# Optimization experiments

Measured on AMD Instinct MI355X. Metric: run time of the kernel, lower is better.

Reference implementation:

```python
import jax, jax.numpy as jnp
import numpy as np

NOISE_EPS = 0.01
TOP_K = 2


def setup_inputs() -> dict:
    key = jax.random.key(0)
    k1, k2, k3, k4 = jax.random.split(key, 4)
    B, S, D, E = 4, 4096, 2048, 64
    x = jax.random.normal(k1, (B, S, D), dtype=jnp.float32)
    raw_noise = jax.random.normal(k2, (B, S, E), dtype=jnp.float32)
    # gating_mlp: single Linear(D -> E), init std=0.02, zero bias
    W_gate = 0.02 * jax.random.normal(k3, (E, D), dtype=jnp.float32)
    b_gate = jnp.zeros((E,), dtype=jnp.float32)
    # noise_projection: Linear(D -> E, bias=False), init std=1/sqrt(D)
    W_noise = (1.0 / np.sqrt(D)) * jax.random.normal(k4, (E, D), dtype=jnp.float32)
    return {"x": x, "raw_noise": raw_noise, "W_gate": W_gate, "b_gate": b_gate, "W_noise": W_noise}


def reference(x, raw_noise, W_gate, b_gate, W_noise):
    # gate logits: [B,S,E]
    logits = jnp.einsum("bsd,ed->bse", x, W_gate) + b_gate
    # noisy top-k routing (training path)
    noise_stddev = jax.nn.softplus(jnp.einsum("bsd,ed->bse", x, W_noise)) + NOISE_EPS
    noisy = logits + raw_noise * noise_stddev
    top_v, top_i = jax.lax.top_k(noisy, TOP_K)            # [B,S,K]
    top_p = jax.nn.softmax(top_v.astype(jnp.float32), axis=-1).astype(noisy.dtype)
    B, S, E = noisy.shape
    T = B * S
    flat_logits = noisy.reshape(T, E)
    flat_i = top_i.reshape(T, TOP_K)
    flat_p = top_p.reshape(T, TOP_K)
    sparse = jnp.zeros((T, E), dtype=noisy.dtype).at[jnp.arange(T)[:, None], flat_i].set(flat_p)
    # aux load-balancing loss
    indicator = (sparse > 0.0).astype(jnp.float32)
    fraction_routed = indicator.sum(axis=0) / T           # f_e
    router_probs = jax.nn.softmax(flat_logits.astype(jnp.float32), axis=-1)
    avg_prob = router_probs.mean(axis=0)                  # p_e
    aux_loss = jnp.sum(fraction_routed * avg_prob) * E
    return sparse.reshape(B, S, E), aux_loss.astype(noisy.dtype)
```

## Files before the change

kernel.cpp:

```cpp
#include <hip/hip_runtime.h>
#include <math.h>

#define TOK 16384
#define DD  2048
#define EE  64
#define MT  32
#define BK  128
#define NKC 8
#define LDA 136
#define XREG (MT * LDA)

typedef _Float16 half4v __attribute__((ext_vector_type(4)));
typedef _Float16 half8  __attribute__((ext_vector_type(8)));
typedef float    floatx4 __attribute__((ext_vector_type(4)));

__global__ void build_wf(const float* __restrict__ Wg, const float* __restrict__ Wn,
                         _Float16* __restrict__ wf) {
  int tid  = blockIdx.x * 256 + threadIdx.x;
  int lane = tid & 63;
  int kc   = (tid >> 6) & 63;
  int ct   = tid >> 12;
  int col  = (ct & 3) * 16 + (lane & 15);
  int k    = kc * 32 + (lane >> 4) * 8;
  const float* W = (ct < 4) ? Wg : Wn;
  const float* src = W + (size_t)col * DD + k;
  float4 a = *reinterpret_cast<const float4*>(src);
  float4 b = *reinterpret_cast<const float4*>(src + 4);
  float v[8] = {a.x, a.y, a.z, a.w, b.x, b.y, b.z, b.w};
  half8 hi, lo;
#pragma unroll
  for (int j = 0; j < 8; ++j) {
    _Float16 h = (_Float16)v[j];
    hi[j] = h;
    lo[j] = (_Float16)(v[j] - (float)h);
  }
  size_t base = (((size_t)(ct * 64 + kc) * 2 + 0) * 64 + lane) * 8;
  *reinterpret_cast<half8*>(wf + base)       = hi;
  *reinterpret_cast<half8*>(wf + base + 512) = lo;
}

#define STAGE(BUF, P0, P1, P2, P3)                                              \
  {                                                                             \
    float4 pav[4] = {P0, P1, P2, P3};                                           \
    _Float16* xh = xs + ((g * 2 + (BUF)) * 2 + 0) * XREG + stok * LDA + skof;   \
    _Float16* xl = xh + XREG;                                                   \
    _Pragma("unroll")                                                           \
    for (int j = 0; j < 4; ++j) {                                               \
      float v[4] = {pav[j].x, pav[j].y, pav[j].z, pav[j].w};                    \
      half4v hi, lo;                                                            \
      _Pragma("unroll")                                                         \
      for (int jj = 0; jj < 4; ++jj) {                                          \
        _Float16 h = (_Float16)v[jj];                                           \
        hi[jj] = h;                                                             \
        lo[jj] = (_Float16)(v[jj] - (float)h);                                  \
      }                                                                         \
      *reinterpret_cast<half4v*>(xh + j * 32) = hi;                             \
      *reinterpret_cast<half4v*>(xl + j * 32) = lo;                             \
    }                                                                           \
  }

#define SUBK(KK, SC, SP, DOPF)                                                  \
  {                                                                             \
    half8 Ah[2], Al[2];                                                         \
    _Pragma("unroll")                                                           \
    for (int mt = 0; mt < 2; ++mt) {                                            \
      Ah[mt] = *reinterpret_cast<const half8*>(xsh + (mt * 16) * LDA + (KK) * 32); \
      Al[mt] = *reinterpret_cast<const half8*>(xsl + (mt * 16) * LDA + (KK) * 32); \
    }                                                                           \
    if (DOPF) {                                                                 \
      const int ck = g * 32 + kc * 4 + (KK) + 1;                                \
      _Pragma("unroll")                                                         \
      for (int nt = 0; nt < 2; ++nt) {                                          \
        const int ct = w4 + nt * 4;                                             \
        _Pragma("unroll")                                                       \
        for (int s = 0; s < 2; ++s)                                             \
          SP[nt][s] = wfp[((size_t)(ct * 64 + ck) * 2 + s) * 64 + l];           \
      }                                                                         \
    }                                                                           \
    _Pragma("unroll")                                                           \
    for (int mt = 0; mt < 2; ++mt)                                              \
      _Pragma("unroll")                                                         \
      for (int nt = 0; nt < 2; ++nt)                                            \
        acc[mt][nt] = __builtin_amdgcn_mfma_f32_16x16x32_f16(Ah[mt], SC[nt][0], acc[mt][nt], 0, 0, 0); \
    _Pragma("unroll")                                                           \
    for (int mt = 0; mt < 2; ++mt)                                              \
      _Pragma("unroll")                                                         \
      for (int nt = 0; nt < 2; ++nt)                                            \
        acc[mt][nt] = __builtin_amdgcn_mfma_f32_16x16x32_f16(Ah[mt], SC[nt][1], acc[mt][nt], 0, 0, 0); \
    _Pragma("unroll")                                                           \
    for (int mt = 0; mt < 2; ++mt)                                              \
      _Pragma("unroll")                                                         \
      for (int nt = 0; nt < 2; ++nt)                                            \
        acc[mt][nt] = __builtin_amdgcn_mfma_f32_16x16x32_f16(Al[mt], SC[nt][0], acc[mt][nt], 0, 0, 0); \
  }

__global__ __launch_bounds__(512, 4)
void gating_kernel(const float* __restrict__ x, const float* __restrict__ rn,
                   const _Float16* __restrict__ wf, const float* __restrict__ bg,
                   float* __restrict__ out,
                   float* __restrict__ cnt_g, float* __restrict__ psum_g) {
  __shared__ char smem[69632];
  _Float16* xs   = (_Float16*)smem;
  float*    Pacc = (float*)smem;
  float*    Vb   = (float*)(smem + 16384);
  float*    Eb   = (float*)(smem + 24832);
  float*    isum = (float*)(smem + 33280);
  int*      ti   = (int*)(smem + 33408);
  float*    tp   = (float*)(smem + 33664);

  const int t  = threadIdx.x;
  const int g  = t >> 8;
  const int tg = t & 255;
  const int w4 = tg >> 6;
  const int l  = t & 63;
  const int q  = l >> 4;
  const int cl = l & 15;
  const int c  = w4 * 16 + cl;
  const int t0 = blockIdx.x * MT;

  const int stok = tg >> 3;
  const int skof = (tg & 7) * 4;
  const float* xrow = x + (size_t)(t0 + stok) * DD + g * (NKC * BK) + skof;

  float bgv = 0.f;
  float rnv[2][4] = {{0.f,0.f,0.f,0.f},{0.f,0.f,0.f,0.f}};
  if (g == 0) {
    bgv = bg[c];
#pragma unroll
    for (int mt = 0; mt < 2; ++mt)
#pragma unroll
      for (int r = 0; r < 4; ++r)
        rnv[mt][r] = rn[(size_t)(t0 + mt * 16 + q * 4 + r) * EE + c];
  }

  floatx4 acc[2][2];
#pragma unroll
  for (int mt = 0; mt < 2; ++mt)
#pragma unroll
    for (int nt = 0; nt < 2; ++nt) acc[mt][nt] = (floatx4)0.f;

  const half8* wfp = (const half8*)wf;
  half8 Bs0[2][2], Bs1[2][2];

  {
    float4 a0 = *reinterpret_cast<const float4*>(xrow);
    float4 a1 = *reinterpret_cast<const float4*>(xrow + 32);
    float4 a2 = *reinterpret_cast<const float4*>(xrow + 64);
    float4 a3 = *reinterpret_cast<const float4*>(xrow + 96);
    STAGE(0, a0, a1, a2, a3)
    const int ck0 = g * 32;
#pragma unroll
    for (int nt = 0; nt < 2; ++nt) {
      const int ct = w4 + nt * 4;
#pragma unroll
      for (int s = 0; s < 2; ++s)
        Bs0[nt][s] = wfp[((size_t)(ct * 64 + ck0) * 2 + s) * 64 + l];
    }
  }

#pragma unroll 2
  for (int kc = 0; kc < NKC; ++kc) {
    const int cur = kc & 1;
    const bool more = (kc < NKC - 1);
    float4 p0, p1, p2, p3;
    if (more) {
      const float* xn = xrow + (kc + 1) * BK;
      p0 = *reinterpret_cast<const float4*>(xn);
      p1 = *reinterpret_cast<const float4*>(xn + 32);
      p2 = *reinterpret_cast<const float4*>(xn + 64);
      p3 = *reinterpret_cast<const float4*>(xn + 96);
    }
    asm volatile("s_waitcnt lgkmcnt(0)" ::: "memory");
    __builtin_amdgcn_s_barrier();

    const _Float16* xsh = xs + ((g * 2 + cur) * 2 + 0) * XREG + cl * LDA + q * 8;
    const _Float16* xsl = xsh + XREG;

    SUBK(0, Bs0, Bs1, 1)
    SUBK(1, Bs1, Bs0, 1)
    SUBK(2, Bs0, Bs1, 1)
    SUBK(3, Bs1, Bs0, more)

    if (more) {
      STAGE(cur ^ 1, p0, p1, p2, p3)
    }
  }

  __syncthreads();

  if (g == 1) {
#pragma unroll
    for (int mt = 0; mt < 2; ++mt)
#pragma unroll
      for (int nt = 0; nt < 2; ++nt)
#pragma unroll
        for (int r = 0; r < 4; ++r)
          Pacc[((((w4 * 2 + mt) * 2 + nt) * 4) + r) * 64 + l] = acc[mt][nt][r];
  }
  __syncthreads();

  if (g == 0) {
#pragma unroll
    for (int mt = 0; mt < 2; ++mt)
#pragma unroll
      for (int nt = 0; nt < 2; ++nt)
#pragma unroll
        for (int r = 0; r < 4; ++r)
          acc[mt][nt][r] += Pacc[((((w4 * 2 + mt) * 2 + nt) * 4) + r) * 64 + l];

#pragma unroll
    for (int mt = 0; mt < 2; ++mt)
#pragma unroll
      for (int r = 0; r < 4; ++r) {
        const int tk = mt * 16 + q * 4 + r;
        float gt = acc[mt][0][r] + bgv;
        float h  = acc[mt][1][r];
        float sp = (h > 20.f) ? h : log1pf(expf(h));
        float v  = gt + rnv[mt][r] * (sp + 0.01f);
        Vb[tk * 66 + c] = v;
        Eb[tk * 66 + c] = expf(v);
      }
  }
  __syncthreads();

  if (t < MT) {
    float v1 = -1e30f, v2 = -1e30f;
    int   i1 = 0, i2 = 0;
    float s = 0.f;
    for (int e = 0; e < EE; ++e) {
      float v = Vb[t * 66 + e];
      s += Eb[t * 66 + e];
      if (v > v1)      { v2 = v1; i2 = i1; v1 = v; i1 = e; }
      else if (v > v2) { v2 = v;  i2 = e; }
    }
    isum[t] = 1.f / s;
    ti[t * 2 + 0] = i1; ti[t * 2 + 1] = i2;
    float e2 = expf(v2 - v1);
    float dn = 1.f + e2;
    tp[t * 2 + 0] = 1.f / dn;
    tp[t * 2 + 1] = e2 / dn;
  }
  __syncthreads();

  {
    const int m  = t >> 4;
    const int c0 = (t & 15) * 4;
    const int i1 = ti[m * 2 + 0], i2 = ti[m * 2 + 1];
    const float p1 = tp[m * 2 + 0], p2 = tp[m * 2 + 1];
    float o[4];
#pragma unroll
    for (int j = 0; j < 4; ++j) {
      const int col = c0 + j;
      o[j] = (col == i1) ? p1 : ((col == i2) ? p2 : 0.f);
    }
    *reinterpret_cast<float4*>(out + (size_t)(t0 + m) * EE + c0) =
        make_float4(o[0], o[1], o[2], o[3]);
  }

  if (t < EE) {
    float s = 0.f;
    int   cn = 0;
#pragma unroll
    for (int m = 0; m < MT; ++m) {
      s  += Eb[m * 66 + t] * isum[m];
      cn += (ti[m * 2 + 0] == t) + (ti[m * 2 + 1] == t);
    }
    atomicAdd(&psum_g[t], s);
    atomicAdd(&cnt_g[t], (float)cn);
  }
}

__global__ void aux_kernel(const float* __restrict__ cnt_g,
                           const float* __restrict__ psum_g,
                           float* __restrict__ out) {
  int e = threadIdx.x;
  float v = cnt_g[e] * psum_g[e];
#pragma unroll
  for (int o = 32; o > 0; o >>= 1) v += __shfl_down(v, o);
  if (e == 0)
    out[(size_t)TOK * EE] = v * ((float)EE / ((float)TOK * (float)TOK));
}

extern "C" void kernel_launch(void* const* d_in, const int* in_sizes, int n_in,
                              void* d_out, int out_size, void* d_ws, size_t ws_size,
                              hipStream_t stream) {
  const float* x  = (const float*)d_in[0];
  const float* rn = (const float*)d_in[1];
  const float* Wg = (const float*)d_in[2];
  const float* bg = (const float*)d_in[3];
  const float* Wn = (const float*)d_in[4];
  float* out    = (float*)d_out;
  float* cnt_g  = (float*)d_ws;
  float* psum_g = cnt_g + EE;
  _Float16* wf  = (_Float16*)((float*)d_ws + 128);

  hipMemsetAsync(d_ws, 0, 2 * EE * sizeof(float), stream);
  build_wf<<<128, 256, 0, stream>>>(Wg, Wn, wf);
  gating_kernel<<<TOK / MT, 512, 0, stream>>>(x, rn, wf, bg, out, cnt_g, psum_g);
  aux_kernel<<<1, 64, 0, stream>>>(cnt_g, psum_g, out);
}
```

Before: 226.9 us.

## Halve token tile to 16 and drop weight register prefetch

Shrinks the per-block token tile from 32 to 16, which doubles the grid size, halves shared memory and raises the launch-bounds occupancy hint to 8. The double-buffered weight-fragment prefetch is replaced by loading the weights inside each sub-k step, and each thread now stages 8 contiguous floats of x. The workspace memset is folded into build_wf to drop a launch. The trade-off is that each block now reads the whole fp16 weight set for half as many tokens, doubling weight traffic, and weight load latency is no longer hidden by the prefetch.

```diff
diff --git a/kernel.cpp b/kernel.cpp
--- a/kernel.cpp
+++ b/kernel.cpp
@@ -4,19 +4,21 @@
 #define TOK 16384
 #define DD  2048
 #define EE  64
-#define MT  32
+#define MT  16
 #define BK  128
 #define NKC 8
 #define LDA 136
 #define XREG (MT * LDA)
+#define NBLK (TOK / MT)
 
 typedef _Float16 half4v __attribute__((ext_vector_type(4)));
 typedef _Float16 half8  __attribute__((ext_vector_type(8)));
 typedef float    floatx4 __attribute__((ext_vector_type(4)));
 
 __global__ void build_wf(const float* __restrict__ Wg, const float* __restrict__ Wn,
-                         _Float16* __restrict__ wf) {
-  int tid  = blockIdx.x * 256 + threadIdx.x;
+                         _Float16* __restrict__ wf, float* __restrict__ zws) {
+  if (blockIdx.x == 0 && threadIdx.x < 128) zws[threadIdx.x] = 0.f;
+  int tid  = blockIdx.x * 128 + threadIdx.x;
   int lane = tid & 63;
   int kc   = (tid >> 6) & 63;
   int ct   = tid >> 12;
@@ -39,13 +41,13 @@
   *reinterpret_cast<half8*>(wf + base + 512) = lo;
 }
 
-#define STAGE(BUF, P0, P1, P2, P3)                                              \
+#define STAGE(BUF, P0, P1)                                                      \
   {                                                                             \
-    float4 pav[4] = {P0, P1, P2, P3};                                           \
+    float4 pav[2] = {P0, P1};                                                   \
     _Float16* xh = xs + ((g * 2 + (BUF)) * 2 + 0) * XREG + stok * LDA + skof;   \
     _Float16* xl = xh + XREG;                                                   \
     _Pragma("unroll")                                                           \
-    for (int j = 0; j < 4; ++j) {                                               \
+    for (int j = 0; j < 2; ++j) {                                               \
       float v[4] = {pav[j].x, pav[j].y, pav[j].z, pav[j].w};                    \
       half4v hi, lo;                                                            \
       _Pragma("unroll")                                                         \
@@ -54,59 +56,48 @@
         hi[jj] = h;                                                             \
         lo[jj] = (_Float16)(v[jj] - (float)h);                                  \
       }                                                                         \
-      *reinterpret_cast<half4v*>(xh + j * 32) = hi;                             \
-      *reinterpret_cast<half4v*>(xl + j * 32) = lo;                             \
+      *reinterpret_cast<half4v*>(xh + j * 4) = hi;                              \
+      *reinterpret_cast<half4v*>(xl + j * 4) = lo;                              \
     }                                                                           \
   }
 
-#define SUBK(KK, SC, SP, DOPF)                                                  \
+#define SUBK(KK)                                                                \
   {                                                                             \
-    half8 Ah[2], Al[2];                                                         \
-    _Pragma("unroll")                                                           \
-    for (int mt = 0; mt < 2; ++mt) {                                            \
-      Ah[mt] = *reinterpret_cast<const half8*>(xsh + (mt * 16) * LDA + (KK) * 32); \
-      Al[mt] = *reinterpret_cast<const half8*>(xsl + (mt * 16) * LDA + (KK) * 32); \
+    half8 Ah = *reinterpret_cast<const half8*>(xsh + (KK) * 32);                \
+    half8 Al = *reinterpret_cast<const half8*>(xsl + (KK) * 32);                \
+    half8 Bv[2][2];                                                             \
+    const int ck = g * 32 + kc * 4 + (KK);                                      \
+    _Pragma("unroll")                                                           \
+    for (int nt = 0; nt < 2; ++nt) {                                            \
+      const int ct = w4 + nt * 4;                                               \
+      _Pragma("unroll")                                                         \
+      for (int s = 0; s < 2; ++s)                                               \
+        Bv[nt][s] = wfp[((size_t)(ct * 64 + ck) * 2 + s) * 64 + l];             \
     }                                                                           \
-    if (DOPF) {                                                                 \
-      const int ck = g * 32 + kc * 4 + (KK) + 1;                                \
-      _Pragma("unroll")                                                         \
-      for (int nt = 0; nt < 2; ++nt) {                                          \
-        const int ct = w4 + nt * 4;                                             \
-        _Pragma("unroll")                                                       \
-        for (int s = 0; s < 2; ++s)                                             \
-          SP[nt][s] = wfp[((size_t)(ct * 64 + ck) * 2 + s) * 64 + l];           \
-      }                                                                         \
-    }                                                                           \
-    _Pragma("unroll")                                                           \
-    for (int mt = 0; mt < 2; ++mt)                                              \
-      _Pragma("unroll")                                                         \
-      for (int nt = 0; nt < 2; ++nt)                                            \
-        acc[mt][nt] = __builtin_amdgcn_mfma_f32_16x16x32_f16(Ah[mt], SC[nt][0], acc[mt][nt], 0, 0, 0); \
-    _Pragma("unroll")                                                           \
-    for (int mt = 0; mt < 2; ++mt)                                              \
-      _Pragma("unroll")                                                         \
-      for (int nt = 0; nt < 2; ++nt)                                            \
-        acc[mt][nt] = __builtin_amdgcn_mfma_f32_16x16x32_f16(Ah[mt], SC[nt][1], acc[mt][nt], 0, 0, 0); \
-    _Pragma("unroll")                                                           \
-    for (int mt = 0; mt < 2; ++mt)                                              \
-      _Pragma("unroll")                                                         \
-      for (int nt = 0; nt < 2; ++nt)                                            \
-        acc[mt][nt] = __builtin_amdgcn_mfma_f32_16x16x32_f16(Al[mt], SC[nt][0], acc[mt][nt], 0, 0, 0); \
-  }
-
-__global__ __launch_bounds__(512, 4)
+    _Pragma("unroll")                                                           \
+    for (int nt = 0; nt < 2; ++nt)                                              \
+      acc[nt] = __builtin_amdgcn_mfma_f32_16x16x32_f16(Ah, Bv[nt][0], acc[nt], 0, 0, 0); \
+    _Pragma("unroll")                                                           \
+    for (int nt = 0; nt < 2; ++nt)                                              \
+      acc[nt] = __builtin_amdgcn_mfma_f32_16x16x32_f16(Ah, Bv[nt][1], acc[nt], 0, 0, 0); \
+    _Pragma("unroll")                                                           \
+    for (int nt = 0; nt < 2; ++nt)                                              \
+      acc[nt] = __builtin_amdgcn_mfma_f32_16x16x32_f16(Al, Bv[nt][0], acc[nt], 0, 0, 0); \
+  }
+
+__global__ __launch_bounds__(512, 8)
 void gating_kernel(const float* __restrict__ x, const float* __restrict__ rn,
                    const _Float16* __restrict__ wf, const float* __restrict__ bg,
                    float* __restrict__ out,
                    float* __restrict__ cnt_g, float* __restrict__ psum_g) {
-  __shared__ char smem[69632];
+  __shared__ char smem[34816];
   _Float16* xs   = (_Float16*)smem;
   float*    Pacc = (float*)smem;
-  float*    Vb   = (float*)(smem + 16384);
-  float*    Eb   = (float*)(smem + 24832);
-  float*    isum = (float*)(smem + 33280);
-  int*      ti   = (int*)(smem + 33408);
-  float*    tp   = (float*)(smem + 33664);
+  float*    Vb   = (float*)(smem + 8192);
+  float*    Eb   = (float*)(smem + 12416);
+  float*    isum = (float*)(smem + 16640);
+  int*      ti   = (int*)(smem + 16704);
+  float*    tp   = (float*)(smem + 16832);
 
   const int t  = threadIdx.x;
   const int g  = t >> 8;
@@ -118,57 +109,31 @@
   const int c  = w4 * 16 + cl;
   const int t0 = blockIdx.x * MT;
 
-  const int stok = tg >> 3;
-  const int skof = (tg & 7) * 4;
+  const int stok = tg >> 4;
+  const int skof = (tg & 15) * 8;
   const float* xrow = x + (size_t)(t0 + stok) * DD + g * (NKC * BK) + skof;
 
-  float bgv = 0.f;
-  float rnv[2][4] = {{0.f,0.f,0.f,0.f},{0.f,0.f,0.f,0.f}};
-  if (g == 0) {
-    bgv = bg[c];
-#pragma unroll
-    for (int mt = 0; mt < 2; ++mt)
-#pragma unroll
-      for (int r = 0; r < 4; ++r)
-        rnv[mt][r] = rn[(size_t)(t0 + mt * 16 + q * 4 + r) * EE + c];
-  }
-
-  floatx4 acc[2][2];
-#pragma unroll
-  for (int mt = 0; mt < 2; ++mt)
-#pragma unroll
-    for (int nt = 0; nt < 2; ++nt) acc[mt][nt] = (floatx4)0.f;
+  floatx4 acc[2];
+  acc[0] = (floatx4)0.f;
+  acc[1] = (floatx4)0.f;
 
   const half8* wfp = (const half8*)wf;
-  half8 Bs0[2][2], Bs1[2][2];
 
   {
     float4 a0 = *reinterpret_cast<const float4*>(xrow);
-    float4 a1 = *reinterpret_cast<const float4*>(xrow + 32);
-    float4 a2 = *reinterpret_cast<const float4*>(xrow + 64);
-    float4 a3 = *reinterpret_cast<const float4*>(xrow + 96);
-    STAGE(0, a0, a1, a2, a3)
-    const int ck0 = g * 32;
-#pragma unroll
-    for (int nt = 0; nt < 2; ++nt) {
-      const int ct = w4 + nt * 4;
-#pragma unroll
-      for (int s = 0; s < 2; ++s)
-        Bs0[nt][s] = wfp[((size_t)(ct * 64 + ck0) * 2 + s) * 64 + l];
-    }
+    float4 a1 = *reinterpret_cast<const float4*>(xrow + 4);
+    STAGE(0, a0, a1)
   }
 
 #pragma unroll 2
   for (int kc = 0; kc < NKC; ++kc) {
     const int cur = kc & 1;
     const bool more = (kc < NKC - 1);
-    float4 p0, p1, p2, p3;
+    float4 p0, p1;
     if (more) {
       const float* xn = xrow + (kc + 1) * BK;
       p0 = *reinterpret_cast<const float4*>(xn);
-      p1 = *reinterpret_cast<const float4*>(xn + 32);
-      p2 = *reinterpret_cast<const float4*>(xn + 64);
-      p3 = *reinterpret_cast<const float4*>(xn + 96);
+      p1 = *reinterpret_cast<const float4*>(xn + 4);
     }
     asm volatile("s_waitcnt lgkmcnt(0)" ::: "memory");
     __builtin_amdgcn_s_barrier();
@@ -176,13 +141,13 @@
     const _Float16* xsh = xs + ((g * 2 + cur) * 2 + 0) * XREG + cl * LDA + q * 8;
     const _Float16* xsl = xsh + XREG;
 
-    SUBK(0, Bs0, Bs1, 1)
-    SUBK(1, Bs1, Bs0, 1)
-    SUBK(2, Bs0, Bs1, 1)
-    SUBK(3, Bs1, Bs0, more)
+    SUBK(0)
+    SUBK(1)
+    SUBK(2)
+    SUBK(3)
 
     if (more) {
-      STAGE(cur ^ 1, p0, p1, p2, p3)
+      STAGE(cur ^ 1, p0, p1)
     }
   }
 
@@ -190,36 +155,36 @@
 
   if (g == 1) {
 #pragma unroll
-    for (int mt = 0; mt < 2; ++mt)
-#pragma unroll
-      for (int nt = 0; nt < 2; ++nt)
-#pragma unroll
-        for (int r = 0; r < 4; ++r)
-          Pacc[((((w4 * 2 + mt) * 2 + nt) * 4) + r) * 64 + l] = acc[mt][nt][r];
+    for (int nt = 0; nt < 2; ++nt)
+#pragma unroll
+      for (int r = 0; r < 4; ++r)
+        Pacc[((w4 * 2 + nt) * 4 + r) * 64 + l] = acc[nt][r];
   }
   __syncthreads();
 
   if (g == 0) {
-#pragma unroll
-    for (int mt = 0; mt < 2; ++mt)
-#pragma unroll
-      for (int nt = 0; nt < 2; ++nt)
-#pragma unroll
-        for (int r = 0; r < 4; ++r)
-          acc[mt][nt][r] += Pacc[((((w4 * 2 + mt) * 2 + nt) * 4) + r) * 64 + l];
-
-#pragma unroll
-    for (int mt = 0; mt < 2; ++mt)
-#pragma unroll
-      for (int r = 0; r < 4; ++r) {
-        const int tk = mt * 16 + q * 4 + r;
-        float gt = acc[mt][0][r] + bgv;
-        float h  = acc[mt][1][r];
-        float sp = (h > 20.f) ? h : log1pf(expf(h));
-        float v  = gt + rnv[mt][r] * (sp + 0.01f);
-        Vb[tk * 66 + c] = v;
-        Eb[tk * 66 + c] = expf(v);
-      }
+    const float bgv = bg[c];
+    float rnv[4];
+#pragma unroll
+    for (int r = 0; r < 4; ++r)
+      rnv[r] = rn[(size_t)(t0 + q * 4 + r) * EE + c];
+
+#pragma unroll
+    for (int nt = 0; nt < 2; ++nt)
+#pragma unroll
+      for (int r = 0; r < 4; ++r)
+        acc[nt][r] += Pacc[((w4 * 2 + nt) * 4 + r) * 64 + l];
+
+#pragma unroll
+    for (int r = 0; r < 4; ++r) {
+      const int tk = q * 4 + r;
+      float gt = acc[0][r] + bgv;
+      float h  = acc[1][r];
+      float sp = (h > 20.f) ? h : log1pf(expf(h));
+      float v  = gt + rnv[r] * (sp + 0.01f);
+      Vb[tk * 66 + c] = v;
+      Eb[tk * 66 + c] = expf(v);
+    }
   }
   __syncthreads();
 
@@ -242,7 +207,7 @@
   }
   __syncthreads();
 
-  {
+  if (t < 256) {
     const int m  = t >> 4;
     const int c0 = (t & 15) * 4;
     const int i1 = ti[m * 2 + 0], i2 = ti[m * 2 + 1];
@@ -292,10 +257,9 @@
   float* out    = (float*)d_out;
   float* cnt_g  = (float*)d_ws;
   float* psum_g = cnt_g + EE;
-  _Float16* wf  = (_Float16*)((float*)d_ws + 128);
-
-  hipMemsetAsync(d_ws, 0, 2 * EE * sizeof(float), stream);
-  build_wf<<<128, 256, 0, stream>>>(Wg, Wn, wf);
-  gating_kernel<<<TOK / MT, 512, 0, stream>>>(x, rn, wf, bg, out, cnt_g, psum_g);
+  _Float16* wf  = (_Float16*)((float*)d_ws + 256);
+
+  build_wf<<<256, 128, 0, stream>>>(Wg, Wn, wf, cnt_g);
+  gating_kernel<<<NBLK, 512, 0, stream>>>(x, rn, wf, bg, out, cnt_g, psum_g);
   aux_kernel<<<1, 64, 0, stream>>>(cnt_g, psum_g, out);
 }
```

After: 243.7 us. 1.07x slower.
